# Performance work log

Hardware: AMD Instinct MI355X
Metric: run time of the kernel (lower is better)

The kernel has to match this reference:

```python
import jax, jax.numpy as jnp
import numpy as np

N_NODES = 100000
N_EDGES = 3200000
F_IN, F_HID, F_OUT = 32, 32, 16


def spline_conv(x, edge_index, edge_attr, W, root, bias):
    """SplineConv, dim=1, kernel_size=2, degree=1, open spline, aggr='mean'.
    Basis weights over the 2 kernel slots are (1-u, u) for pseudo u in [0,1).
    W: [2, Fin, Fout], root: [Fin, Fout], bias: [Fout]."""
    src, dst = edge_index[0], edge_index[1]
    u = jnp.clip(edge_attr[:, 0:1], 0.0, 1.0)          # [E,1]
    x_src = x[src]                                      # [E,Fin] gather
    msg = (1.0 - u) * (x_src @ W[0]) + u * (x_src @ W[1])  # [E,Fout]
    agg = jax.ops.segment_sum(msg, dst, num_segments=x.shape[0])
    cnt = jax.ops.segment_sum(jnp.ones((msg.shape[0],), dtype=x.dtype), dst,
                              num_segments=x.shape[0])
    agg = agg / jnp.maximum(cnt, 1.0)[:, None]          # mean aggregation
    return agg + x @ root + bias


def setup_inputs() -> dict:
    key = jax.random.key(0)
    ks = jax.random.split(key, 9)
    x = jax.random.normal(ks[0], (N_NODES, F_IN), dtype=jnp.float32)
    edge_index = jax.random.randint(ks[1], (2, N_EDGES), 0, N_NODES, dtype=jnp.int64)
    edge_attr = jax.random.uniform(ks[2], (N_EDGES, 1), dtype=jnp.float32)
    s1 = 1.0 / np.sqrt(F_IN)
    s2 = 1.0 / np.sqrt(F_HID)
    W1 = jax.random.normal(ks[3], (2, F_IN, F_HID), dtype=jnp.float32) * s1
    root1 = jax.random.normal(ks[4], (F_IN, F_HID), dtype=jnp.float32) * s1
    b1 = jnp.zeros((F_HID,), dtype=jnp.float32)
    W2 = jax.random.normal(ks[5], (2, F_HID, F_OUT), dtype=jnp.float32) * s2
    root2 = jax.random.normal(ks[6], (F_HID, F_OUT), dtype=jnp.float32) * s2
    b2 = jnp.zeros((F_OUT,), dtype=jnp.float32)
    return {"x": x, "edge_index": edge_index, "edge_attr": edge_attr,
            "W1": W1, "root1": root1, "b1": b1,
            "W2": W2, "root2": root2, "b2": b2}


def reference(x, edge_index, edge_attr, W1, root1, b1, W2, root2, b2):
    # dropout is identity in eval mode
    h = jax.nn.relu(spline_conv(x, edge_index, edge_attr, W1, root1, b1))
    h = spline_conv(h, edge_index, edge_attr, W2, root2, b2)
    return jax.nn.log_softmax(h, axis=1)
```

## Files before the change

kernel.cpp:

```cpp
#include <hip/hip_runtime.h>
#include <math.h>

#define NN 100000
#define NE 3200000
#define BSH 6
#define BSZ 64
#define NBKT 1563
#define CAP 2560
#define STILE 8192
#define NTBS 391
#define TST 68

#define FMA4(a, s, v) { (a).x += (s)*(v).x; (a).y += (s)*(v).y; (a).z += (s)*(v).z; (a).w += (s)*(v).w; }

__device__ __forceinline__ unsigned bf16rn(float f) {
    unsigned u = __float_as_uint(f);
    return (u + 0x7fffu + ((u >> 16) & 1u)) >> 16;
}
__device__ __forceinline__ float blo(unsigned w) { return __uint_as_float(w << 16); }
__device__ __forceinline__ float bhi(unsigned w) { return __uint_as_float(w & 0xffff0000u); }

__global__ __launch_bounds__(512) void scatter_k(const int* __restrict__ ei, const float* __restrict__ ea,
                                                 int* __restrict__ bcur, int* __restrict__ pk) {
    __shared__ int h[NBKT];
    __shared__ int base[NBKT];
    int t = threadIdx.x;
    for (int j = t; j < NBKT; j += 512) h[j] = 0;
    __syncthreads();
    int e0 = blockIdx.x * STILE + t;
    unsigned pck[16]; int bk[16], rk[16];
    #pragma unroll
    for (int i = 0; i < 16; i++) {
        int e = e0 + i * 512;
        bk[i] = -1;
        if (e < NE) {
            int s = ei[e];
            int d = ei[NE + e];
            float u = fminf(fmaxf(ea[e], 0.f), 1.f);
            unsigned uq = __float2uint_rn(u * 511.f);
            bk[i] = d >> BSH;
            pck[i] = ((unsigned)s << 15) | ((unsigned)(d & (BSZ - 1)) << 9) | uq;
            rk[i] = atomicAdd(&h[bk[i]], 1);
        }
    }
    __syncthreads();
    for (int j = t; j < NBKT; j += 512) base[j] = h[j] ? atomicAdd(&bcur[j], h[j]) : 0;
    __syncthreads();
    #pragma unroll
    for (int i = 0; i < 16; i++) {
        if (bk[i] >= 0) {
            int p = base[bk[i]] + rk[i];
            if (p < CAP) pk[(size_t)bk[i] * CAP + p] = (int)pck[i];
        }
    }
}

__global__ __launch_bounds__(256) void prep1_k(
    const float* __restrict__ x, const float* __restrict__ R, const float* __restrict__ b,
    unsigned* __restrict__ xb, float* __restrict__ xr)
{
    __shared__ float Rs[1024];
    __shared__ float xs[32 * 33];
    int t = threadIdx.x;
    for (int i = t; i < 1024; i += 256) Rs[i] = R[i];
    int nb = blockIdx.x * 32;
    for (int i = t; i < 1024; i += 256) {
        int n = nb + (i >> 5);
        xs[(i >> 5) * 33 + (i & 31)] = (n < NN) ? x[n * 32 + (i & 31)] : 0.f;
    }
    __syncthreads();
    int local = t >> 3, c = t & 7;
    int n = nb + local;
    float4 a2 = make_float4(0.f, 0.f, 0.f, 0.f);
    #pragma unroll
    for (int k = 0; k < 32; k++) {
        float xk = xs[local * 33 + k];
        float4 r = ((const float4*)Rs)[k * 8 + c];
        FMA4(a2, xk, r);
    }
    if (n < NN) {
        float4 bb = ((const float4*)b)[c];
        a2.x += bb.x; a2.y += bb.y; a2.z += bb.z; a2.w += bb.w;
        ((float4*)xr)[n * 8 + c] = a2;
        float f0 = xs[local * 33 + c * 4 + 0];
        float f1 = xs[local * 33 + c * 4 + 1];
        float f2 = xs[local * 33 + c * 4 + 2];
        float f3 = xs[local * 33 + c * 4 + 3];
        uint2 pkd;
        pkd.x = bf16rn(f0) | (bf16rn(f1) << 16);
        pkd.y = bf16rn(f2) | (bf16rn(f3) << 16);
        ((uint2*)xb)[n * 8 + c] = pkd;
    }
}

__global__ __launch_bounds__(256) void agg1_k(
    const int* __restrict__ bcur, const int* __restrict__ pk,
    const unsigned* __restrict__ xb, const float* __restrict__ W,
    const float* __restrict__ xr, unsigned* __restrict__ hb)
{
    __shared__ float Wc[2048];
    __shared__ int ccnt[BSZ], coff[BSZ];
    __shared__ __align__(16) char smraw[BSZ * TST * 4];
    int* pks = (int*)smraw;
    float* tb = (float*)smraw;

    int t = threadIdx.x;
    for (int i = t; i < 1024; i += 256) {
        float w0 = W[i];
        Wc[i] = w0;
        Wc[1024 + i] = W[1024 + i] - w0;
    }
    if (t < BSZ) ccnt[t] = 0;
    __syncthreads();

    int bkt = blockIdx.x;
    int ne = bcur[bkt]; if (ne > CAP) ne = CAP;
    const int* sp = pk + (size_t)bkt * CAP;

    unsigned er[10]; int rk[10];
    #pragma unroll
    for (int i = 0; i < 10; i++) {
        int e = i * 256 + t;
        rk[i] = -1;
        if (e < ne) {
            er[i] = (unsigned)sp[e];
            rk[i] = atomicAdd(&ccnt[(er[i] >> 9) & (BSZ - 1)], 1);
        }
    }
    __syncthreads();
    if (t < BSZ) {
        int v = ccnt[t], sc = v;
        #pragma unroll
        for (int ofs = 1; ofs < 64; ofs <<= 1) {
            int nn = __shfl_up(sc, ofs);
            if (t >= ofs) sc += nn;
        }
        coff[t] = sc - v;
    }
    __syncthreads();
    #pragma unroll
    for (int i = 0; i < 10; i++)
        if (rk[i] >= 0) pks[coff[(er[i] >> 9) & (BSZ - 1)] + rk[i]] = (int)er[i];
    __syncthreads();

    int r = t >> 2, j = t & 3;
    int cs = coff[r], cn = ccnt[r];
    const uint4* x4 = (const uint4*)xb;
    uint4 zz = make_uint4(0, 0, 0, 0);
    float T[8] = {0,0,0,0,0,0,0,0}, B[8] = {0,0,0,0,0,0,0,0};
    unsigned p0 = 0, p1 = 0; uint4 v0 = zz, v1 = zz;
    if (cn > 0) { p0 = (unsigned)pks[cs];     v0 = x4[(size_t)(p0 >> 15) * 4 + j]; }
    if (cn > 1) { p1 = (unsigned)pks[cs + 1]; v1 = x4[(size_t)(p1 >> 15) * 4 + j]; }
    for (int k = 0; k < cn; k++) {
        unsigned p2 = 0; uint4 v2 = zz;
        if (k + 2 < cn) { p2 = (unsigned)pks[cs + k + 2]; v2 = x4[(size_t)(p2 >> 15) * 4 + j]; }
        float u = (float)(p0 & 511u) * (1.f / 511.f);
        float f0 = blo(v0.x), f1 = bhi(v0.x), f2 = blo(v0.y), f3 = bhi(v0.y);
        float f4 = blo(v0.z), f5 = bhi(v0.z), f6 = blo(v0.w), f7 = bhi(v0.w);
        T[0] += f0; B[0] += u * f0;  T[1] += f1; B[1] += u * f1;
        T[2] += f2; B[2] += u * f2;  T[3] += f3; B[3] += u * f3;
        T[4] += f4; B[4] += u * f4;  T[5] += f5; B[5] += u * f5;
        T[6] += f6; B[6] += u * f6;  T[7] += f7; B[7] += u * f7;
        p0 = p1; v0 = v1; p1 = p2; v1 = v2;
    }
    __syncthreads();

    ((float4*)(tb + r * TST + 8 * j))[0]      = make_float4(T[0], T[1], T[2], T[3]);
    ((float4*)(tb + r * TST + 8 * j))[1]      = make_float4(T[4], T[5], T[6], T[7]);
    ((float4*)(tb + r * TST + 32 + 8 * j))[0] = make_float4(B[0], B[1], B[2], B[3]);
    ((float4*)(tb + r * TST + 32 + 8 * j))[1] = make_float4(B[4], B[5], B[6], B[7]);
    __syncthreads();

    #pragma unroll
    for (int r0 = 0; r0 < BSZ; r0 += 32) {
        int row = r0 + (t >> 3), cc = t & 7;
        int n = bkt * BSZ + row;
        float inv = 1.f / fmaxf((float)ccnt[row], 1.f);
        float4 acc = make_float4(0.f, 0.f, 0.f, 0.f);
        #pragma unroll
        for (int k = 0; k < 32; k++) {
            float sa = tb[row * TST + k];
            float4 w = ((const float4*)Wc)[k * 8 + cc];
            FMA4(acc, sa, w);
        }
        #pragma unroll
        for (int k = 0; k < 32; k++) {
            float sb = tb[row * TST + 32 + k];
            float4 w = ((const float4*)Wc)[(32 + k) * 8 + cc];
            FMA4(acc, sb, w);
        }
        if (n < NN) {
            float4 rr = ((const float4*)xr)[n * 8 + cc];
            float h0 = fmaxf(acc.x * inv + rr.x, 0.f);
            float h1 = fmaxf(acc.y * inv + rr.y, 0.f);
            float h2 = fmaxf(acc.z * inv + rr.z, 0.f);
            float h3 = fmaxf(acc.w * inv + rr.w, 0.f);
            uint2 pkd;
            pkd.x = bf16rn(h0) | (bf16rn(h1) << 16);
            pkd.y = bf16rn(h2) | (bf16rn(h3) << 16);
            ((uint2*)hb)[n * 8 + cc] = pkd;
        }
    }
}

__global__ __launch_bounds__(256) void prep2_k(
    const unsigned* __restrict__ hb, const float* __restrict__ R, const float* __restrict__ b,
    float* __restrict__ hr)
{
    __shared__ float Rs[512];
    __shared__ float xs[64 * 33];
    int t = threadIdx.x;
    for (int i = t; i < 512; i += 256) Rs[i] = R[i];
    int nb = blockIdx.x * 64;
    for (int i = t; i < 1024; i += 256) {
        int n = nb + (i >> 4), j = i & 15;
        unsigned v = (n < NN) ? hb[n * 16 + j] : 0u;
        xs[(i >> 4) * 33 + 2 * j]     = blo(v);
        xs[(i >> 4) * 33 + 2 * j + 1] = bhi(v);
    }
    __syncthreads();
    int local = t >> 2, c = t & 3;
    int n = nb + local;
    float4 a = make_float4(0.f, 0.f, 0.f, 0.f);
    #pragma unroll
    for (int k = 0; k < 32; k++) {
        float xk = xs[local * 33 + k];
        float4 r = ((const float4*)Rs)[k * 4 + c];
        FMA4(a, xk, r);
    }
    if (n < NN) {
        float4 bb = ((const float4*)b)[c];
        a.x += bb.x; a.y += bb.y; a.z += bb.z; a.w += bb.w;
        ((float4*)hr)[n * 4 + c] = a;
    }
}

__global__ __launch_bounds__(256) void agg2_k(
    const int* __restrict__ bcur, const int* __restrict__ pk,
    const unsigned* __restrict__ hb, const float* __restrict__ W,
    const float* __restrict__ hr, float* __restrict__ out)
{
    __shared__ float Wc[1024];
    __shared__ int ccnt[BSZ], coff[BSZ];
    __shared__ __align__(16) char smraw[BSZ * TST * 4];
    int* pks = (int*)smraw;
    float* tb = (float*)smraw;

    int t = threadIdx.x;
    for (int i = t; i < 512; i += 256) {
        float w0 = W[i];
        Wc[i] = w0;
        Wc[512 + i] = W[512 + i] - w0;
    }
    if (t < BSZ) ccnt[t] = 0;
    __syncthreads();

    int bkt = blockIdx.x;
    int ne = bcur[bkt]; if (ne > CAP) ne = CAP;
    const int* sp = pk + (size_t)bkt * CAP;

    unsigned er[10]; int rk[10];
    #pragma unroll
    for (int i = 0; i < 10; i++) {
        int e = i * 256 + t;
        rk[i] = -1;
        if (e < ne) {
            er[i] = (unsigned)sp[e];
            rk[i] = atomicAdd(&ccnt[(er[i] >> 9) & (BSZ - 1)], 1);
        }
    }
    __syncthreads();
    if (t < BSZ) {
        int v = ccnt[t], sc = v;
        #pragma unroll
        for (int ofs = 1; ofs < 64; ofs <<= 1) {
            int nn = __shfl_up(sc, ofs);
            if (t >= ofs) sc += nn;
        }
        coff[t] = sc - v;
    }
    __syncthreads();
    #pragma unroll
    for (int i = 0; i < 10; i++)
        if (rk[i] >= 0) pks[coff[(er[i] >> 9) & (BSZ - 1)] + rk[i]] = (int)er[i];
    __syncthreads();

    int r = t >> 2, j = t & 3;
    int cs = coff[r], cn = ccnt[r];
    const uint4* x4 = (const uint4*)hb;
    uint4 zz = make_uint4(0, 0, 0, 0);
    float T[8] = {0,0,0,0,0,0,0,0}, B[8] = {0,0,0,0,0,0,0,0};
    unsigned p0 = 0, p1 = 0; uint4 v0 = zz, v1 = zz;
    if (cn > 0) { p0 = (unsigned)pks[cs];     v0 = x4[(size_t)(p0 >> 15) * 4 + j]; }
    if (cn > 1) { p1 = (unsigned)pks[cs + 1]; v1 = x4[(size_t)(p1 >> 15) * 4 + j]; }
    for (int k = 0; k < cn; k++) {
        unsigned p2 = 0; uint4 v2 = zz;
        if (k + 2 < cn) { p2 = (unsigned)pks[cs + k + 2]; v2 = x4[(size_t)(p2 >> 15) * 4 + j]; }
        float u = (float)(p0 & 511u) * (1.f / 511.f);
        float f0 = blo(v0.x), f1 = bhi(v0.x), f2 = blo(v0.y), f3 = bhi(v0.y);
        float f4 = blo(v0.z), f5 = bhi(v0.z), f6 = blo(v0.w), f7 = bhi(v0.w);
        T[0] += f0; B[0] += u * f0;  T[1] += f1; B[1] += u * f1;
        T[2] += f2; B[2] += u * f2;  T[3] += f3; B[3] += u * f3;
        T[4] += f4; B[4] += u * f4;  T[5] += f5; B[5] += u * f5;
        T[6] += f6; B[6] += u * f6;  T[7] += f7; B[7] += u * f7;
        p0 = p1; v0 = v1; p1 = p2; v1 = v2;
    }
    __syncthreads();

    ((float4*)(tb + r * TST + 8 * j))[0]      = make_float4(T[0], T[1], T[2], T[3]);
    ((float4*)(tb + r * TST + 8 * j))[1]      = make_float4(T[4], T[5], T[6], T[7]);
    ((float4*)(tb + r * TST + 32 + 8 * j))[0] = make_float4(B[0], B[1], B[2], B[3]);
    ((float4*)(tb + r * TST + 32 + 8 * j))[1] = make_float4(B[4], B[5], B[6], B[7]);
    __syncthreads();

    #pragma unroll
    for (int r0 = 0; r0 < BSZ; r0 += 16) {
        int row = r0 + (t >> 4), f = t & 15;
        int n = bkt * BSZ + row;
        float inv = 1.f / fmaxf((float)ccnt[row], 1.f);
        float o = 0.f;
        #pragma unroll
        for (int k = 0; k < 32; k++) o += tb[row * TST + k] * Wc[k * 16 + f];
        #pragma unroll
        for (int k = 0; k < 32; k++) o += tb[row * TST + 32 + k] * Wc[(32 + k) * 16 + f];
        if (n < NN) {
            o = o * inv + hr[n * 16 + f];
            float m = o;
            #pragma unroll
            for (int ofs = 8; ofs; ofs >>= 1) m = fmaxf(m, __shfl_xor(m, ofs, 16));
            float sm = expf(o - m);
            #pragma unroll
            for (int ofs = 8; ofs; ofs >>= 1) sm += __shfl_xor(sm, ofs, 16);
            out[n * 16 + f] = o - (m + logf(sm));
        }
    }
}

extern "C" void kernel_launch(void* const* d_in, const int* in_sizes, int n_in,
                              void* d_out, int out_size, void* d_ws, size_t ws_size,
                              hipStream_t stream) {
    const float* x     = (const float*)d_in[0];
    const int*   ei    = (const int*)d_in[1];
    const float* ea    = (const float*)d_in[2];
    const float* W1    = (const float*)d_in[3];
    const float* root1 = (const float*)d_in[4];
    const float* b1    = (const float*)d_in[5];
    const float* W2    = (const float*)d_in[6];
    const float* root2 = (const float*)d_in[7];
    const float* b2    = (const float*)d_in[8];
    float* out = (float*)d_out;

    int* ws = (int*)d_ws;
    int* bcur = ws;
    int* pk   = ws + 2048;
    size_t off = 2048 + (size_t)NBKT * CAP;
    unsigned* xb = (unsigned*)(ws + off);
    unsigned* hb = xb + (size_t)NN * 16;
    float* xr = (float*)(hb + (size_t)NN * 16);
    float* hr = xr + (size_t)NN * 32;

    hipMemsetAsync(bcur, 0, NBKT * sizeof(int), stream);

    scatter_k<<<NTBS, 512, 0, stream>>>(ei, ea, bcur, pk);
    prep1_k  <<<(NN + 31) / 32, 256, 0, stream>>>(x, root1, b1, xb, xr);
    agg1_k   <<<NBKT, 256, 0, stream>>>(bcur, pk, xb, W1, xr, hb);
    prep2_k  <<<(NN + 63) / 64, 256, 0, stream>>>(hb, root2, b2, hr);
    agg2_k   <<<NBKT, 256, 0, stream>>>(bcur, pk, hb, W2, hr, out);
}
```

Measured before the change: 248.2 us.

## Fuse layer-2 root transform into agg1 and widen aggregation blocks to 512 threads

Removes the separate prep2 kernel by computing h@root2+b2 inside agg1_k from the freshly produced hidden rows held in shared memory. This saves one launch and a re-read of hb. Both aggregation kernels now use 512 threads per bucket, with 8 threads per node each gathering 8 bytes instead of 4 threads gathering 16 bytes, and a prefetch depth of 3. This is meant to give more parallelism and more loads in flight on the gather. The cost is extra shared memory and registers per block, plus smaller per-thread loads.

```diff
diff --git a/kernel.cpp b/kernel.cpp
--- a/kernel.cpp
+++ b/kernel.cpp
@@ -93,23 +93,27 @@
     }
 }
 
-__global__ __launch_bounds__(256) void agg1_k(
+__global__ __launch_bounds__(512, 6) void agg1_k(
     const int* __restrict__ bcur, const int* __restrict__ pk,
     const unsigned* __restrict__ xb, const float* __restrict__ W,
-    const float* __restrict__ xr, unsigned* __restrict__ hb)
+    const float* __restrict__ R2, const float* __restrict__ b2,
+    const float* __restrict__ xr, unsigned* __restrict__ hb, float* __restrict__ hr)
 {
     __shared__ float Wc[2048];
+    __shared__ float R2s[512];
     __shared__ int ccnt[BSZ], coff[BSZ];
     __shared__ __align__(16) char smraw[BSZ * TST * 4];
+    __shared__ float hs[BSZ * 33];
     int* pks = (int*)smraw;
     float* tb = (float*)smraw;
 
     int t = threadIdx.x;
-    for (int i = t; i < 1024; i += 256) {
+    for (int i = t; i < 1024; i += 512) {
         float w0 = W[i];
         Wc[i] = w0;
         Wc[1024 + i] = W[1024 + i] - w0;
     }
+    if (t < 512) R2s[t] = R2[t];
     if (t < BSZ) ccnt[t] = 0;
     __syncthreads();
 
@@ -117,10 +121,10 @@
     int ne = bcur[bkt]; if (ne > CAP) ne = CAP;
     const int* sp = pk + (size_t)bkt * CAP;
 
-    unsigned er[10]; int rk[10];
-    #pragma unroll
-    for (int i = 0; i < 10; i++) {
-        int e = i * 256 + t;
+    unsigned er[5]; int rk[5];
+    #pragma unroll
+    for (int i = 0; i < 5; i++) {
+        int e = i * 512 + t;
         rk[i] = -1;
         if (e < ne) {
             er[i] = (unsigned)sp[e];
@@ -139,41 +143,36 @@
     }
     __syncthreads();
     #pragma unroll
-    for (int i = 0; i < 10; i++)
+    for (int i = 0; i < 5; i++)
         if (rk[i] >= 0) pks[coff[(er[i] >> 9) & (BSZ - 1)] + rk[i]] = (int)er[i];
     __syncthreads();
 
-    int r = t >> 2, j = t & 3;
+    int r = t >> 3, j = t & 7;
     int cs = coff[r], cn = ccnt[r];
-    const uint4* x4 = (const uint4*)xb;
-    uint4 zz = make_uint4(0, 0, 0, 0);
-    float T[8] = {0,0,0,0,0,0,0,0}, B[8] = {0,0,0,0,0,0,0,0};
-    unsigned p0 = 0, p1 = 0; uint4 v0 = zz, v1 = zz;
-    if (cn > 0) { p0 = (unsigned)pks[cs];     v0 = x4[(size_t)(p0 >> 15) * 4 + j]; }
-    if (cn > 1) { p1 = (unsigned)pks[cs + 1]; v1 = x4[(size_t)(p1 >> 15) * 4 + j]; }
+    const uint2* x2 = (const uint2*)xb;
+    uint2 zz = make_uint2(0, 0);
+    float T[4] = {0,0,0,0}, B[4] = {0,0,0,0};
+    unsigned p0 = 0, p1 = 0, p2 = 0; uint2 v0 = zz, v1 = zz, v2 = zz;
+    if (cn > 0) { p0 = (unsigned)pks[cs];     v0 = x2[(size_t)(p0 >> 15) * 8 + j]; }
+    if (cn > 1) { p1 = (unsigned)pks[cs + 1]; v1 = x2[(size_t)(p1 >> 15) * 8 + j]; }
+    if (cn > 2) { p2 = (unsigned)pks[cs + 2]; v2 = x2[(size_t)(p2 >> 15) * 8 + j]; }
     for (int k = 0; k < cn; k++) {
-        unsigned p2 = 0; uint4 v2 = zz;
-        if (k + 2 < cn) { p2 = (unsigned)pks[cs + k + 2]; v2 = x4[(size_t)(p2 >> 15) * 4 + j]; }
+        unsigned p3 = 0; uint2 v3 = zz;
+        if (k + 3 < cn) { p3 = (unsigned)pks[cs + k + 3]; v3 = x2[(size_t)(p3 >> 15) * 8 + j]; }
         float u = (float)(p0 & 511u) * (1.f / 511.f);
         float f0 = blo(v0.x), f1 = bhi(v0.x), f2 = blo(v0.y), f3 = bhi(v0.y);
-        float f4 = blo(v0.z), f5 = bhi(v0.z), f6 = blo(v0.w), f7 = bhi(v0.w);
         T[0] += f0; B[0] += u * f0;  T[1] += f1; B[1] += u * f1;
         T[2] += f2; B[2] += u * f2;  T[3] += f3; B[3] += u * f3;
-        T[4] += f4; B[4] += u * f4;  T[5] += f5; B[5] += u * f5;
-        T[6] += f6; B[6] += u * f6;  T[7] += f7; B[7] += u * f7;
-        p0 = p1; v0 = v1; p1 = p2; v1 = v2;
-    }
-    __syncthreads();
-
-    ((float4*)(tb + r * TST + 8 * j))[0]      = make_float4(T[0], T[1], T[2], T[3]);
-    ((float4*)(tb + r * TST + 8 * j))[1]      = make_float4(T[4], T[5], T[6], T[7]);
-    ((float4*)(tb + r * TST + 32 + 8 * j))[0] = make_float4(B[0], B[1], B[2], B[3]);
-    ((float4*)(tb + r * TST + 32 + 8 * j))[1] = make_float4(B[4], B[5], B[6], B[7]);
-    __syncthreads();
-
-    #pragma unroll
-    for (int r0 = 0; r0 < BSZ; r0 += 32) {
-        int row = r0 + (t >> 3), cc = t & 7;
+        p0 = p1; v0 = v1; p1 = p2; v1 = v2; p2 = p3; v2 = v3;
+    }
+    __syncthreads();
+
+    ((float4*)(tb + r * TST + 4 * j))[0]      = make_float4(T[0], T[1], T[2], T[3]);
+    ((float4*)(tb + r * TST + 32 + 4 * j))[0] = make_float4(B[0], B[1], B[2], B[3]);
+    __syncthreads();
+
+    {
+        int row = t >> 3, cc = t & 7;
         int n = bkt * BSZ + row;
         float inv = 1.f / fmaxf((float)ccnt[row], 1.f);
         float4 acc = make_float4(0.f, 0.f, 0.f, 0.f);
@@ -189,53 +188,40 @@
             float4 w = ((const float4*)Wc)[(32 + k) * 8 + cc];
             FMA4(acc, sb, w);
         }
+        float h0 = 0.f, h1 = 0.f, h2 = 0.f, h3 = 0.f;
         if (n < NN) {
             float4 rr = ((const float4*)xr)[n * 8 + cc];
-            float h0 = fmaxf(acc.x * inv + rr.x, 0.f);
-            float h1 = fmaxf(acc.y * inv + rr.y, 0.f);
-            float h2 = fmaxf(acc.z * inv + rr.z, 0.f);
-            float h3 = fmaxf(acc.w * inv + rr.w, 0.f);
+            h0 = fmaxf(acc.x * inv + rr.x, 0.f);
+            h1 = fmaxf(acc.y * inv + rr.y, 0.f);
+            h2 = fmaxf(acc.z * inv + rr.z, 0.f);
+            h3 = fmaxf(acc.w * inv + rr.w, 0.f);
             uint2 pkd;
             pkd.x = bf16rn(h0) | (bf16rn(h1) << 16);
             pkd.y = bf16rn(h2) | (bf16rn(h3) << 16);
             ((uint2*)hb)[n * 8 + cc] = pkd;
         }
-    }
-}
-
-__global__ __launch_bounds__(256) void prep2_k(
-    const unsigned* __restrict__ hb, const float* __restrict__ R, const float* __restrict__ b,
-    float* __restrict__ hr)
-{
-    __shared__ float Rs[512];
-    __shared__ float xs[64 * 33];
-    int t = threadIdx.x;
-    for (int i = t; i < 512; i += 256) Rs[i] = R[i];
-    int nb = blockIdx.x * 64;
-    for (int i = t; i < 1024; i += 256) {
-        int n = nb + (i >> 4), j = i & 15;
-        unsigned v = (n < NN) ? hb[n * 16 + j] : 0u;
-        xs[(i >> 4) * 33 + 2 * j]     = blo(v);
-        xs[(i >> 4) * 33 + 2 * j + 1] = bhi(v);
-    }
-    __syncthreads();
-    int local = t >> 2, c = t & 3;
-    int n = nb + local;
-    float4 a = make_float4(0.f, 0.f, 0.f, 0.f);
-    #pragma unroll
-    for (int k = 0; k < 32; k++) {
-        float xk = xs[local * 33 + k];
-        float4 r = ((const float4*)Rs)[k * 4 + c];
-        FMA4(a, xk, r);
-    }
-    if (n < NN) {
-        float4 bb = ((const float4*)b)[c];
-        a.x += bb.x; a.y += bb.y; a.z += bb.z; a.w += bb.w;
-        ((float4*)hr)[n * 4 + c] = a;
-    }
-}
-
-__global__ __launch_bounds__(256) void agg2_k(
+        hs[row * 33 + cc * 4 + 0] = h0;
+        hs[row * 33 + cc * 4 + 1] = h1;
+        hs[row * 33 + cc * 4 + 2] = h2;
+        hs[row * 33 + cc * 4 + 3] = h3;
+    }
+    __syncthreads();
+
+    #pragma unroll
+    for (int p = 0; p < 2; p++) {
+        int idx = p * 512 + t;
+        int row = idx >> 4, f = idx & 15;
+        int n = bkt * BSZ + row;
+        if (n < NN) {
+            float o = 0.f;
+            #pragma unroll
+            for (int k = 0; k < 32; k++) o += hs[row * 33 + k] * R2s[k * 16 + f];
+            hr[n * 16 + f] = o + b2[f];
+        }
+    }
+}
+
+__global__ __launch_bounds__(512, 6) void agg2_k(
     const int* __restrict__ bcur, const int* __restrict__ pk,
     const unsigned* __restrict__ hb, const float* __restrict__ W,
     const float* __restrict__ hr, float* __restrict__ out)
@@ -247,10 +233,10 @@
     float* tb = (float*)smraw;
 
     int t = threadIdx.x;
-    for (int i = t; i < 512; i += 256) {
-        float w0 = W[i];
-        Wc[i] = w0;
-        Wc[512 + i] = W[512 + i] - w0;
+    if (t < 512) {
+        float w0 = W[t];
+        Wc[t] = w0;
+        Wc[512 + t] = W[512 + t] - w0;
     }
     if (t < BSZ) ccnt[t] = 0;
     __syncthreads();
@@ -259,10 +245,10 @@
     int ne = bcur[bkt]; if (ne > CAP) ne = CAP;
     const int* sp = pk + (size_t)bkt * CAP;
 
-    unsigned er[10]; int rk[10];
-    #pragma unroll
-    for (int i = 0; i < 10; i++) {
-        int e = i * 256 + t;
+    unsigned er[5]; int rk[5];
+    #pragma unroll
+    for (int i = 0; i < 5; i++) {
+        int e = i * 512 + t;
         rk[i] = -1;
         if (e < ne) {
             er[i] = (unsigned)sp[e];
@@ -281,41 +267,37 @@
     }
     __syncthreads();
     #pragma unroll
-    for (int i = 0; i < 10; i++)
+    for (int i = 0; i < 5; i++)
         if (rk[i] >= 0) pks[coff[(er[i] >> 9) & (BSZ - 1)] + rk[i]] = (int)er[i];
     __syncthreads();
 
-    int r = t >> 2, j = t & 3;
+    int r = t >> 3, j = t & 7;
     int cs = coff[r], cn = ccnt[r];
-    const uint4* x4 = (const uint4*)hb;
-    uint4 zz = make_uint4(0, 0, 0, 0);
-    float T[8] = {0,0,0,0,0,0,0,0}, B[8] = {0,0,0,0,0,0,0,0};
-    unsigned p0 = 0, p1 = 0; uint4 v0 = zz, v1 = zz;
-    if (cn > 0) { p0 = (unsigned)pks[cs];     v0 = x4[(size_t)(p0 >> 15) * 4 + j]; }
-    if (cn > 1) { p1 = (unsigned)pks[cs + 1]; v1 = x4[(size_t)(p1 >> 15) * 4 + j]; }
+    const uint2* x2 = (const uint2*)hb;
+    uint2 zz = make_uint2(0, 0);
+    float T[4] = {0,0,0,0}, B[4] = {0,0,0,0};
+    unsigned p0 = 0, p1 = 0, p2 = 0; uint2 v0 = zz, v1 = zz, v2 = zz;
+    if (cn > 0) { p0 = (unsigned)pks[cs];     v0 = x2[(size_t)(p0 >> 15) * 8 + j]; }
+    if (cn > 1) { p1 = (unsigned)pks[cs + 1]; v1 = x2[(size_t)(p1 >> 15) * 8 + j]; }
+    if (cn > 2) { p2 = (unsigned)pks[cs + 2]; v2 = x2[(size_t)(p2 >> 15) * 8 + j]; }
     for (int k = 0; k < cn; k++) {
-        unsigned p2 = 0; uint4 v2 = zz;
-        if (k + 2 < cn) { p2 = (unsigned)pks[cs + k + 2]; v2 = x4[(size_t)(p2 >> 15) * 4 + j]; }
+        unsigned p3 = 0; uint2 v3 = zz;
+        if (k + 3 < cn) { p3 = (unsigned)pks[cs + k + 3]; v3 = x2[(size_t)(p3 >> 15) * 8 + j]; }
         float u = (float)(p0 & 511u) * (1.f / 511.f);
         float f0 = blo(v0.x), f1 = bhi(v0.x), f2 = blo(v0.y), f3 = bhi(v0.y);
-        float f4 = blo(v0.z), f5 = bhi(v0.z), f6 = blo(v0.w), f7 = bhi(v0.w);
         T[0] += f0; B[0] += u * f0;  T[1] += f1; B[1] += u * f1;
         T[2] += f2; B[2] += u * f2;  T[3] += f3; B[3] += u * f3;
-        T[4] += f4; B[4] += u * f4;  T[5] += f5; B[5] += u * f5;
-        T[6] += f6; B[6] += u * f6;  T[7] += f7; B[7] += u * f7;
-        p0 = p1; v0 = v1; p1 = p2; v1 = v2;
-    }
-    __syncthreads();
-
-    ((float4*)(tb + r * TST + 8 * j))[0]      = make_float4(T[0], T[1], T[2], T[3]);
-    ((float4*)(tb + r * TST + 8 * j))[1]      = make_float4(T[4], T[5], T[6], T[7]);
-    ((float4*)(tb + r * TST + 32 + 8 * j))[0] = make_float4(B[0], B[1], B[2], B[3]);
-    ((float4*)(tb + r * TST + 32 + 8 * j))[1] = make_float4(B[4], B[5], B[6], B[7]);
-    __syncthreads();
-
-    #pragma unroll
-    for (int r0 = 0; r0 < BSZ; r0 += 16) {
-        int row = r0 + (t >> 4), f = t & 15;
+        p0 = p1; v0 = v1; p1 = p2; v1 = v2; p2 = p3; v2 = v3;
+    }
+    __syncthreads();
+
+    ((float4*)(tb + r * TST + 4 * j))[0]      = make_float4(T[0], T[1], T[2], T[3]);
+    ((float4*)(tb + r * TST + 32 + 4 * j))[0] = make_float4(B[0], B[1], B[2], B[3]);
+    __syncthreads();
+
+    #pragma unroll
+    for (int p = 0; p < 2; p++) {
+        int row = p * 32 + (t >> 4), f = t & 15;
         int n = bkt * BSZ + row;
         float inv = 1.f / fmaxf((float)ccnt[row], 1.f);
         float o = 0.f;
@@ -363,7 +345,6 @@
 
     scatter_k<<<NTBS, 512, 0, stream>>>(ei, ea, bcur, pk);
     prep1_k  <<<(NN + 31) / 32, 256, 0, stream>>>(x, root1, b1, xb, xr);
-    agg1_k   <<<NBKT, 256, 0, stream>>>(bcur, pk, xb, W1, xr, hb);
-    prep2_k  <<<(NN + 63) / 64, 256, 0, stream>>>(hb, root2, b2, hr);
-    agg2_k   <<<NBKT, 256, 0, stream>>>(bcur, pk, hb, W2, hr, out);
-}
+    agg1_k   <<<NBKT, 512, 0, stream>>>(bcur, pk, xb, W1, root2, b2, xr, hb, hr);
+    agg2_k   <<<NBKT, 512, 0, stream>>>(bcur, pk, hb, W2, hr, out);
+}
```

Result: faster. 239.3 us (-3.6%).
